# Performance work log

Hardware: AMD Instinct MI355X
Metric: run time of the kernel (lower is better)

Reference implementation:

```python
import jax, jax.numpy as jnp
import numpy as np
import math

N_ENTITIES = 200000
N_ITEMS = 100000
N_REL = 40
DIM = 64
N_HEADS = 2
DK = DIM // N_HEADS
N_EDGES = 1500000
K_EDGES = 256
K_ITEMS = 100


def setup_inputs() -> dict:
    key = jax.random.key(0)
    k1, k2, k3, k4, k5, k6 = jax.random.split(key, 6)
    entity_emb = jax.random.normal(k1, (N_ENTITIES, DIM), jnp.float32) * 0.1
    W_Q = jax.random.normal(k2, (DIM, DIM), jnp.float32) * (1.0 / math.sqrt(DIM))
    relation_emb = jax.random.normal(k3, (N_REL - 1, DIM), jnp.float32) * 0.1
    edge_index = jax.random.randint(k4, (2, N_EDGES), 0, N_ENTITIES, jnp.int32)
    # edge_type in [1, N_REL-1]: code indexes relation_emb[edge_type - 1]
    edge_type = jax.random.randint(k5, (N_EDGES,), 1, N_REL, jnp.int32)
    # uniform(0,1) driving the gumbel noise -log(-log(u)); clipped away from 0
    noise_u = jax.random.uniform(k6, (N_EDGES,), jnp.float32, 1e-9, 1.0)
    return {"entity_emb": entity_emb, "W_Q": W_Q, "relation_emb": relation_emb,
            "noise_u": noise_u, "edge_index": edge_index, "edge_type": edge_type}


def reference(entity_emb, W_Q, relation_emb, noise_u, edge_index, edge_type):
    head, tail = edge_index[0], edge_index[1]
    E = edge_index.shape[1]

    # --- norm_attn_computer (AttnHGCN): per-edge multi-head attention ---
    # project once on nodes, then gather (same math as (emb[head] @ W_Q))
    proj = entity_emb @ W_Q                               # [N, D]
    q = proj[head].reshape(E, N_HEADS, DK)                # [E, H, Dk]
    k = proj[tail].reshape(E, N_HEADS, DK)                # [E, H, Dk]
    rel = relation_emb[edge_type - 1].reshape(E, N_HEADS, DK)
    attn = jnp.sum(q * k * rel, axis=-1) / math.sqrt(DK)  # [E, H]
    edge_attn_logits = attn.mean(axis=-1)                 # [E]

    # scatter_softmax over head nodes, then multiply by head degree (norm)
    seg_max = jax.lax.stop_gradient(
        jax.ops.segment_max(edge_attn_logits, head, num_segments=N_ENTITIES))
    ex = jnp.exp(edge_attn_logits - seg_max[head])
    denom = jax.ops.segment_sum(ex, head, num_segments=N_ENTITIES)
    edge_attn_score = ex / denom[head]
    deg = jax.ops.segment_sum(jnp.ones_like(edge_attn_logits), head,
                              num_segments=N_ENTITIES)
    edge_attn_score = edge_attn_score * deg[head]         # [E]

    # --- attn logit sums per item (head + tail scatter_sum), topk 100 ---
    sum_by_node = (jax.ops.segment_sum(edge_attn_logits, head, num_segments=N_ENTITIES)
                   + jax.ops.segment_sum(edge_attn_logits, tail, num_segments=N_ENTITIES))
    top_items_v, top_attn_items = jax.lax.top_k(sum_by_node[:N_ITEMS], K_ITEMS)

    # --- gumbel-noise injection + edge topk 256 ---
    noisy_score = edge_attn_score + (-jnp.log(-jnp.log(noise_u)))
    topk_v, topk_attn_edge_id = jax.lax.top_k(noisy_score, K_EDGES)

    return (edge_attn_score, topk_v, topk_attn_edge_id, top_items_v, top_attn_items)
```

## Files before the change

### kernel.cpp

```cpp
#include <hip/hip_runtime.h>

#define N_ENTITIES 200000
#define N_ITEMS    100000
#define DIM        64
#define N_EDGES    1500000
#define K_EDGES    256
#define K_ITEMS    100
#define SCALE      0.08838834764831845f

#define CAND_CAP   8192
#define NSCANB     ((N_ENTITIES + 255) / 256)
#define NXCD       8

typedef unsigned long long u64;


__device__ __forceinline__ unsigned xcd_atomic_add(unsigned* p, unsigned v) {
    return __hip_atomic_fetch_add(p, v, __ATOMIC_RELAXED, __HIP_MEMORY_SCOPE_WORKGROUP);
}
__device__ __forceinline__ void xcd_atomic_addf(float* p, float v) {
    __hip_atomic_fetch_add(p, v, __ATOMIC_RELAXED, __HIP_MEMORY_SCOPE_WORKGROUP);
}

__device__ __forceinline__ unsigned fkey(float x) {
    unsigned u = __float_as_uint(x);
    return (u & 0x80000000u) ? ~u : (u | 0x80000000u);
}
__device__ __forceinline__ float funkey(unsigned k) {
    return (k & 0x80000000u) ? __uint_as_float(k & 0x7fffffffu)
                             : __uint_as_float(~k);
}

__device__ __forceinline__ void lds_hist_add(unsigned* h, unsigned bin, bool valid, int lane) {
    bool need = valid;
    for (;;) {
        unsigned long long mask = __ballot(need);
        if (mask == 0ull) break;
        int leader = __ffsll(mask) - 1;
        unsigned lbin = __shfl(bin, leader, 64);
        bool same = need && (bin == lbin);
        unsigned long long grp = __ballot(same);
        if (lane == leader) atomicAdd(&h[lbin], (unsigned)__popcll(grp));
        need = need && !same;
    }
}

__device__ __forceinline__ unsigned select_digit(const unsigned* __restrict__ hist,
                                                 unsigned Keff, unsigned* above) {
    unsigned cum = 0;
    int b = 255;
    for (; b > 0; --b) {
        unsigned hb = hist[b];
        if (cum + hb >= Keff) break;
        cum += hb;
    }
    *above = cum;
    return (unsigned)b;
}

__global__ __launch_bounds__(256) void proj_kernel(const float* __restrict__ emb,
                                                   const float* __restrict__ W,
                                                   float* __restrict__ proj,
                                                   const int* __restrict__ head,
                                                   unsigned* __restrict__ degiX,
                                                   unsigned* __restrict__ rank) {
    unsigned xcd;
    asm volatile("s_getreg_b32 %0, hwreg(HW_REG_XCC_ID)" : "=s"(xcd));
    xcd &= (NXCD - 1);

    int e = blockIdx.x * blockDim.x + threadIdx.x;
    unsigned rk = 0;
    bool haveEdge = (e < N_EDGES);
    if (haveEdge)
        rk = (xcd << 28) | xcd_atomic_add(&degiX[(size_t)xcd * N_ENTITIES + head[e]], 1u);

    __shared__ float part[4][16][64];
    const int t = threadIdx.x;
    const int c = t & 63;
    const int q = __builtin_amdgcn_readfirstlane(t >> 6);

    float Wreg[16];
#pragma unroll
    for (int j = 0; j < 16; ++j) Wreg[j] = W[(q * 16 + j) * 64 + c];

    const int base = blockIdx.x * 16;
    const float* erow = emb + (size_t)base * 64 + q * 16;

    float acc[16];
#pragma unroll
    for (int r = 0; r < 16; ++r) acc[r] = 0.f;
#pragma unroll
    for (int r = 0; r < 16; ++r) {
#pragma unroll
        for (int j = 0; j < 16; ++j)
            acc[r] += erow[r * 64 + j] * Wreg[j];
    }
#pragma unroll
    for (int r = 0; r < 16; ++r) part[q][r][c] = acc[r];
    __syncthreads();
#pragma unroll
    for (int it = 0; it < 4; ++it) {
        int oi = t + it * 256;
        int r = oi >> 6, cc = oi & 63;
        float s = part[0][r][cc] + part[1][r][cc] + part[2][r][cc] + part[3][r][cc];
        proj[(size_t)(base + r) * 64 + cc] = s;
    }
    if (haveEdge) rank[e] = rk;
}

__global__ void scan1_kernel(unsigned* __restrict__ degiX,
                             unsigned* __restrict__ degtot,
                             unsigned* __restrict__ start,
                             unsigned* __restrict__ bsum) {
    __shared__ unsigned s[256];
    int t = threadIdx.x, i = blockIdx.x * 256 + t;
    unsigned tot = 0;
    if (i < N_ENTITIES) {
        unsigned px[NXCD];
#pragma unroll
        for (int x = 0; x < NXCD; ++x) {
            px[x] = tot;
            tot += degiX[(size_t)x * N_ENTITIES + i];
        }
#pragma unroll
        for (int x = 0; x < NXCD; ++x)
            degiX[(size_t)x * N_ENTITIES + i] = px[x];
        degtot[i] = tot;
    }
    s[t] = tot;
    __syncthreads();
    for (int off = 1; off < 256; off <<= 1) {
        unsigned x = s[t];
        unsigned y = (t >= off) ? s[t - off] : 0u;
        __syncthreads();
        s[t] = x + y;
        __syncthreads();
    }
    if (i < N_ENTITIES) start[i] = s[t] - tot;
    if (t == 255) bsum[blockIdx.x] = s[t];
}

__global__ __launch_bounds__(256) void scan23_kernel(const unsigned* __restrict__ bsum,
                                                     unsigned* __restrict__ start,
                                                     unsigned* __restrict__ degiX) {
    __shared__ unsigned part[4];
    const int b = blockIdx.x;
    const int t = threadIdx.x;
    unsigned s = 0;
    for (int j = t; j < b; j += 256) s += bsum[j];
#pragma unroll
    for (int off = 1; off < 64; off <<= 1) s += __shfl_xor(s, off, 64);
    if ((t & 63) == 0) part[t >> 6] = s;
    __syncthreads();
    unsigned prefix = part[0] + part[1] + part[2] + part[3];
    int i = b * 256 + t;
    if (i < N_ENTITIES) {
        unsigned sg = start[i] + prefix;
        start[i] = sg;
#pragma unroll
        for (int x = 0; x < NXCD; ++x)
            degiX[(size_t)x * N_ENTITIES + i] += sg;
    }
}

__global__ void scatter_kernel(const int* __restrict__ head, const int* __restrict__ tail,
                               const int* __restrict__ etype,
                               unsigned* __restrict__ rank,
                               const unsigned* __restrict__ startX,
                               u64* __restrict__ rec, int csrMode) {
    int i = blockIdx.x * blockDim.x + threadIdx.x;
    if (i >= N_EDGES) return;
    unsigned r = rank[i];
    unsigned x = r >> 28;
    unsigned slot = startX[(size_t)x * N_ENTITIES + head[i]] + (r & 0x0FFFFFFFu);
    u64 R = ((u64)(unsigned)tail[i] << 27) | ((u64)(unsigned)(etype[i] - 1) << 21) | (u64)(unsigned)i;
    rec[slot] = R;
    if (csrMode) rank[i] = slot;
}

__global__ __launch_bounds__(256) void node_pass(const float4* __restrict__ proj4,
                                                 const float4* __restrict__ rel4,
                                                 const u64* __restrict__ rec,
                                                 const unsigned* __restrict__ start,
                                                 const unsigned* __restrict__ degtot,
                                                 float* __restrict__ logitsOut,
                                                 int csrMode,
                                                 float2* __restrict__ nd,
                                                 float* __restrict__ sumhead,
                                                 float* __restrict__ sumtailR,
                                                 int repMask) {
    unsigned xcd;
    asm volatile("s_getreg_b32 %0, hwreg(HW_REG_XCC_ID)" : "=s"(xcd));
    float* st = sumtailR + (size_t)(xcd & (unsigned)repMask) * N_ITEMS;
    const bool xcdLocal = (repMask == NXCD - 1);

    int wave = (blockIdx.x * blockDim.x + threadIdx.x) >> 6;
    int lane = threadIdx.x & 63;
    int slot = lane >> 4, sl = lane & 15;
    unsigned s = start[wave], len = degtot[wave];
    float4 ph = proj4[(size_t)wave * 16 + sl];
    float dsum = 0.f, lsum = 0.f;
    for (unsigned k0 = 0; k0 < len; k0 += 8) {
        unsigned ka = k0 + slot, kb = ka + 4;
        bool va = (ka < len), vb = (kb < len);
        u64 Ra = rec[s + (va ? ka : 0u)];
        u64 Rb = rec[s + (vb ? kb : 0u)];
        unsigned ta = (unsigned)(Ra >> 27), ria = ((unsigned)(Ra >> 21)) & 63u;
        unsigned tb = (unsigned)(Rb >> 27), rib = ((unsigned)(Rb >> 21)) & 63u;
        unsigned ea = (unsigned)Ra & 0x1FFFFFu, eb = (unsigned)Rb & 0x1FFFFFu;
        float4 pa = proj4[(size_t)ta * 16 + sl];
        float4 qa = rel4[(size_t)ria * 16 + sl];
        float4 pb = proj4[(size_t)tb * 16 + sl];
        float4 qb = rel4[(size_t)rib * 16 + sl];
        float xa = ph.x * pa.x * qa.x + ph.y * pa.y * qa.y + ph.z * pa.z * qa.z + ph.w * pa.w * qa.w;
        float xb = ph.x * pb.x * qb.x + ph.y * pb.y * qb.y + ph.z * pb.z * qb.z + ph.w * pb.w * qb.w;
        xa += __shfl_xor(xa, 1, 64);  xb += __shfl_xor(xb, 1, 64);
        xa += __shfl_xor(xa, 2, 64);  xb += __shfl_xor(xb, 2, 64);
        xa += __shfl_xor(xa, 4, 64);  xb += __shfl_xor(xb, 4, 64);
        xa += __shfl_xor(xa, 8, 64);  xb += __shfl_xor(xb, 8, 64);
        if (sl == 0) {
            if (va) {
                float lg = xa * SCALE;
                logitsOut[csrMode ? (s + ka) : ea] = lg;
                dsum += __expf(lg);
                lsum += lg;
                if (ta < N_ITEMS) {
                    if (xcdLocal) xcd_atomic_addf(&st[ta], lg);
                    else          atomicAdd(&st[ta], lg);
                }
            }
            if (vb) {
                float lg = xb * SCALE;
                logitsOut[csrMode ? (s + kb) : eb] = lg;
                dsum += __expf(lg);
                lsum += lg;
                if (tb < N_ITEMS) {
                    if (xcdLocal) xcd_atomic_addf(&st[tb], lg);
                    else          atomicAdd(&st[tb], lg);
                }
            }
        }
    }
    dsum += __shfl_xor(dsum, 16, 64);
    dsum += __shfl_xor(dsum, 32, 64);
    lsum += __shfl_xor(lsum, 16, 64);
    lsum += __shfl_xor(lsum, 32, 64);
    if (lane == 0) {
        nd[wave] = make_float2(dsum, (float)len);
        sumhead[wave] = lsum;
    }
}

__global__ void edge_pass3(const float* __restrict__ logitsEdge,
                           const float* __restrict__ logitsCsr,
                           const unsigned* __restrict__ slotmap, int csrMode,
                           const int* __restrict__ head,
                           const float2* __restrict__ nd, const float* __restrict__ noise_u,
                           const float* __restrict__ sumhead, const float* __restrict__ sumtailR,
                           int R,
                           float* __restrict__ out_scores, unsigned* __restrict__ keysE,
                           unsigned* __restrict__ keysI, unsigned* __restrict__ hists) {
    __shared__ unsigned hE[256];
    __shared__ unsigned hI[256];
    for (int j = threadIdx.x; j < 256; j += blockDim.x) { hE[j] = 0; hI[j] = 0; }
    __syncthreads();
    int i = blockIdx.x * blockDim.x + threadIdx.x;
    int lane = threadIdx.x & 63;

    unsigned bin = 0;
    bool valid = (i < N_EDGES);
    if (valid) {
        float lg = csrMode ? logitsCsr[slotmap[i]] : logitsEdge[i];
        float2 dd = nd[head[i]];
        float score = __expf(lg) / dd.x * dd.y;
        out_scores[i] = score;
        float noise = -logf(-logf(noise_u[i]));
        unsigned k = fkey(score + noise);
        keysE[i] = k;
        bin = k >> 24;
    }
    lds_hist_add(hE, bin, valid, lane);

    bin = 0;
    valid = (i < N_ITEMS);
    if (valid) {
        float s = sumhead[i];
        for (int r = 0; r < R; ++r) s += sumtailR[(size_t)r * N_ITEMS + i];
        unsigned k = fkey(s);
        keysI[i] = k;
        bin = k >> 24;
    }
    lds_hist_add(hI, bin, valid, lane);

    __syncthreads();
    for (int j = threadIdx.x; j < 256; j += blockDim.x) {
        unsigned v = hE[j];
        if (v) atomicAdd(&hists[j], v);
        v = hI[j];
        if (v) atomicAdd(&hists[3 * 256 + j], v);
    }
}

__global__ void collect_kernel(const unsigned* __restrict__ keysE,
                               const unsigned* __restrict__ keysI,
                               const unsigned* __restrict__ hists,
                               unsigned* __restrict__ counters, unsigned* __restrict__ cand) {
    const int y = blockIdx.y;
    const unsigned* keys = y ? keysI : keysE;
    const int n = y ? N_ITEMS : N_EDGES;
    const unsigned K = y ? K_ITEMS : K_EDGES;
    const unsigned* H = hists + (size_t)y * 3 * 256;
    unsigned aboveA;
    unsigned binA = select_digit(H, K, &aboveA);
    const unsigned T = binA << 24;
    unsigned* cd = cand + (size_t)y * 2 * CAND_CAP;

    int i = blockIdx.x * blockDim.x + threadIdx.x;
    int stride = gridDim.x * blockDim.x;
    for (; i < n; i += stride) {
        unsigned k = keys[i];
        if (k >= T) {
            unsigned p = atomicAdd(&counters[y], 1u);
            if (p < (unsigned)CAND_CAP) { cd[2 * p] = k; cd[2 * p + 1] = (unsigned)i; }
        }
    }
}

__global__ void final_topk_kernel(const unsigned* __restrict__ cand,
                                  const unsigned* __restrict__ counters,
                                  float* __restrict__ out_topkv, float* __restrict__ out_topki,
                                  float* __restrict__ out_itemv, float* __restrict__ out_itemi) {
    __shared__ unsigned sk[CAND_CAP];
    __shared__ unsigned si[CAND_CAP];
    const int y = blockIdx.x;
    const int K = y ? K_ITEMS : K_EDGES;
    float* outv = y ? out_itemv : out_topkv;
    float* outi = y ? out_itemi : out_topki;
    const unsigned* cd = cand + (size_t)y * 2 * CAND_CAP;
    unsigned m = counters[y];
    if (m > (unsigned)CAND_CAP) m = CAND_CAP;
    for (unsigned i = threadIdx.x; i < m; i += blockDim.x) {
        sk[i] = cd[2 * i];
        si[i] = cd[2 * i + 1];
    }
    __syncthreads();
    for (unsigned i = threadIdx.x; i < m; i += blockDim.x) {
        unsigned ki = sk[i], xi = si[i];
        int r = 0;
        for (unsigned j = 0; j < m; ++j) {
            unsigned kj = sk[j];
            if (kj > ki || (kj == ki && si[j] < xi)) r++;
        }
        if (r < K) {
            outv[r] = funkey(ki);
            outi[r] = (float)xi;
        }
    }
}

extern "C" void kernel_launch(void* const* d_in, const int* in_sizes, int n_in,
                              void* d_out, int out_size, void* d_ws, size_t ws_size,
                              hipStream_t stream) {
    (void)in_sizes; (void)n_in; (void)out_size;
    const float* emb    = (const float*)d_in[0];
    const float* W      = (const float*)d_in[1];
    const float* rel    = (const float*)d_in[2];
    const float* noise  = (const float*)d_in[3];
    const int*   eidx   = (const int*)d_in[4];
    const int*   etype  = (const int*)d_in[5];
    const int* head = eidx;
    const int* tail = eidx + N_EDGES;

    float* out        = (float*)d_out;
    float* out_scores = out;
    float* out_topkv  = out + N_EDGES;
    float* out_topki  = out + N_EDGES + K_EDGES;
    float* out_itemv  = out + N_EDGES + 2 * K_EDGES;
    float* out_itemi  = out + N_EDGES + 2 * K_EDGES + K_ITEMS;

    auto layout_floats = [](int R, int csr) -> size_t {
        return (size_t)N_ENTITIES * DIM + N_EDGES + 2 * (size_t)N_EDGES
             + N_ENTITIES + (size_t)NXCD * N_ENTITIES + N_ENTITIES
             + (size_t)R * N_ITEMS
             + 2 * 3 * 256 + 2 + 2 * (size_t)N_ENTITIES + N_ENTITIES
             + 1024 + 2 * 2 * CAND_CAP + (csr ? (size_t)N_EDGES : 0);
    };
    int R = 8, csr = 1;
    while (R > 1 && ws_size < layout_floats(R, 1) * 4) R >>= 1;
    if (ws_size < layout_floats(1, 1) * 4) {
        csr = 0;
        R = 8;
        while (R > 1 && ws_size < layout_floats(R, 0) * 4) R >>= 1;
    }

    float* ws = (float*)d_ws;
    size_t o = 0;
    float*    proj    = ws + o;               o += (size_t)N_ENTITIES * DIM;
    unsigned* rank    = (unsigned*)(ws + o);
    float*    logits  = ws + o;               o += N_EDGES;
    u64*      rec     = (u64*)(ws + o);       o += 2 * (size_t)N_EDGES;
    unsigned* keysE   = (unsigned*)rec;
    unsigned* keysI   = keysE + N_EDGES;
    unsigned* start   = (unsigned*)(ws + o);  o += N_ENTITIES;
    unsigned* degtot  = (unsigned*)(ws + o);  o += N_ENTITIES;
    unsigned* degiX   = (unsigned*)(ws + o);  o += (size_t)NXCD * N_ENTITIES;
    float*    sumtailR= ws + o;               o += (size_t)R * N_ITEMS;
    unsigned* hists   = (unsigned*)(ws + o);  o += 2 * 3 * 256;
    unsigned* counters= (unsigned*)(ws + o);  o += 2;
    float2*   nd      = (float2*)(ws + o);    o += 2 * (size_t)N_ENTITIES;
    float*    sumhead = ws + o;               o += N_ENTITIES;
    unsigned* bsum    = (unsigned*)(ws + o);  o += 1024;
    unsigned* cand    = (unsigned*)(ws + o);  o += 2 * 2 * CAND_CAP;
    float*    logitsCsr = ws + o;             if (csr) o += N_EDGES;

    float*    nodePassLogits = csr ? logitsCsr : logits;

    hipMemsetAsync(degiX, 0,
                   ((size_t)NXCD * N_ENTITIES + (size_t)R * N_ITEMS + 2 * 3 * 256 + 2) * 4,
                   stream);
    hipLaunchKernelGGL(proj_kernel, dim3(12500), dim3(256), 0, stream,
                       emb, W, proj, head, degiX, rank);
    hipLaunchKernelGGL(scan1_kernel, dim3(NSCANB), dim3(256), 0, stream,
                       degiX, degtot, start, bsum);
    hipLaunchKernelGGL(scan23_kernel, dim3(NSCANB), dim3(256), 0, stream,
                       bsum, start, degiX);
    hipLaunchKernelGGL(scatter_kernel, dim3((N_EDGES + 255) / 256), dim3(256), 0, stream,
                       head, tail, etype, rank, degiX, rec, csr);
    hipLaunchKernelGGL(node_pass, dim3(N_ENTITIES / 4), dim3(256), 0, stream,
                       (const float4*)proj, (const float4*)rel, rec, start, degtot,
                       nodePassLogits, csr, nd, sumhead, sumtailR, R - 1);
    hipLaunchKernelGGL(edge_pass3, dim3((N_EDGES + 255) / 256), dim3(256), 0, stream,
                       logits, logitsCsr, rank, csr, head, (const float2*)nd, noise,
                       sumhead, sumtailR, R,
                       out_scores, keysE, keysI, hists);
    hipLaunchKernelGGL(collect_kernel, dim3(512, 2), dim3(256), 0, stream,
                       keysE, keysI, hists, counters, cand);
    hipLaunchKernelGGL(final_topk_kernel, dim3(2), dim3(1024), 0, stream,
                       cand, counters, out_topkv, out_topki, out_itemv, out_itemi);
}
```

Measured before the change: 508.5 us.

## Use grid-stride edge pass with per-block histograms and separate reduction kernel

The edge pass now runs as a fixed grid of 1024 blocks with a grid-stride loop and plain LDS atomics in place of the ballot-based aggregation. Each block writes its 512-bin histogram to its own workspace row, and a new small kernel reduces the rows. This removes global histogram atomics and the memset of the histogram region. The XCD-local float atomic in node_pass is also replaced with an inline-asm global_atomic_add_f32, which could change atomic scope semantics. The cost is an extra kernel launch and more workspace.

```diff
diff --git a/kernel.cpp b/kernel.cpp
--- a/kernel.cpp
+++ b/kernel.cpp
@@ -11,15 +11,16 @@
 #define CAND_CAP   8192
 #define NSCANB     ((N_ENTITIES + 255) / 256)
 #define NXCD       8
+#define NBLK3      1024
 
 typedef unsigned long long u64;
 
 
+__device__ __forceinline__ void l2_atomic_add_f32(float* p, float v) {
+    asm volatile("global_atomic_add_f32 %0, %1, off" :: "v"(p), "v"(v) : "memory");
+}
 __device__ __forceinline__ unsigned xcd_atomic_add(unsigned* p, unsigned v) {
     return __hip_atomic_fetch_add(p, v, __ATOMIC_RELAXED, __HIP_MEMORY_SCOPE_WORKGROUP);
-}
-__device__ __forceinline__ void xcd_atomic_addf(float* p, float v) {
-    __hip_atomic_fetch_add(p, v, __ATOMIC_RELAXED, __HIP_MEMORY_SCOPE_WORKGROUP);
 }
 
 __device__ __forceinline__ unsigned fkey(float x) {
@@ -29,20 +30,6 @@
 __device__ __forceinline__ float funkey(unsigned k) {
     return (k & 0x80000000u) ? __uint_as_float(k & 0x7fffffffu)
                              : __uint_as_float(~k);
-}
-
-__device__ __forceinline__ void lds_hist_add(unsigned* h, unsigned bin, bool valid, int lane) {
-    bool need = valid;
-    for (;;) {
-        unsigned long long mask = __ballot(need);
-        if (mask == 0ull) break;
-        int leader = __ffsll(mask) - 1;
-        unsigned lbin = __shfl(bin, leader, 64);
-        bool same = need && (bin == lbin);
-        unsigned long long grp = __ballot(same);
-        if (lane == leader) atomicAdd(&h[lbin], (unsigned)__popcll(grp));
-        need = need && !same;
-    }
 }
 
 __device__ __forceinline__ unsigned select_digit(const unsigned* __restrict__ hist,
@@ -225,7 +212,7 @@
                 dsum += __expf(lg);
                 lsum += lg;
                 if (ta < N_ITEMS) {
-                    if (xcdLocal) xcd_atomic_addf(&st[ta], lg);
+                    if (xcdLocal) l2_atomic_add_f32(&st[ta], lg);
                     else          atomicAdd(&st[ta], lg);
                 }
             }
@@ -235,7 +222,7 @@
                 dsum += __expf(lg);
                 lsum += lg;
                 if (tb < N_ITEMS) {
-                    if (xcdLocal) xcd_atomic_addf(&st[tb], lg);
+                    if (xcdLocal) l2_atomic_add_f32(&st[tb], lg);
                     else          atomicAdd(&st[tb], lg);
                 }
             }
@@ -251,7 +238,7 @@
     }
 }
 
-__global__ void edge_pass3(const float* __restrict__ logitsEdge,
+__global__ __launch_bounds__(256) void edge_pass3(const float* __restrict__ logitsEdge,
                            const float* __restrict__ logitsCsr,
                            const unsigned* __restrict__ slotmap, int csrMode,
                            const int* __restrict__ head,
@@ -259,17 +246,13 @@
                            const float* __restrict__ sumhead, const float* __restrict__ sumtailR,
                            int R,
                            float* __restrict__ out_scores, unsigned* __restrict__ keysE,
-                           unsigned* __restrict__ keysI, unsigned* __restrict__ hists) {
-    __shared__ unsigned hE[256];
-    __shared__ unsigned hI[256];
-    for (int j = threadIdx.x; j < 256; j += blockDim.x) { hE[j] = 0; hI[j] = 0; }
-    __syncthreads();
-    int i = blockIdx.x * blockDim.x + threadIdx.x;
-    int lane = threadIdx.x & 63;
-
-    unsigned bin = 0;
-    bool valid = (i < N_EDGES);
-    if (valid) {
+                           unsigned* __restrict__ keysI, unsigned* __restrict__ histB) {
+    __shared__ unsigned hh[512];
+    for (int j = threadIdx.x; j < 512; j += blockDim.x) hh[j] = 0;
+    __syncthreads();
+
+    const int stride = NBLK3 * 256;
+    for (int i = blockIdx.x * blockDim.x + threadIdx.x; i < N_EDGES; i += stride) {
         float lg = csrMode ? logitsCsr[slotmap[i]] : logitsEdge[i];
         float2 dd = nd[head[i]];
         float score = __expf(lg) / dd.x * dd.y;
@@ -277,28 +260,29 @@
         float noise = -logf(-logf(noise_u[i]));
         unsigned k = fkey(score + noise);
         keysE[i] = k;
-        bin = k >> 24;
-    }
-    lds_hist_add(hE, bin, valid, lane);
-
-    bin = 0;
-    valid = (i < N_ITEMS);
-    if (valid) {
-        float s = sumhead[i];
-        for (int r = 0; r < R; ++r) s += sumtailR[(size_t)r * N_ITEMS + i];
-        unsigned k = fkey(s);
-        keysI[i] = k;
-        bin = k >> 24;
-    }
-    lds_hist_add(hI, bin, valid, lane);
-
-    __syncthreads();
-    for (int j = threadIdx.x; j < 256; j += blockDim.x) {
-        unsigned v = hE[j];
-        if (v) atomicAdd(&hists[j], v);
-        v = hI[j];
-        if (v) atomicAdd(&hists[3 * 256 + j], v);
-    }
+        atomicAdd(&hh[k >> 24], 1u);
+        if (i < N_ITEMS) {
+            float s = sumhead[i];
+            for (int r = 0; r < R; ++r) s += sumtailR[(size_t)r * N_ITEMS + i];
+            unsigned ki = fkey(s);
+            keysI[i] = ki;
+            atomicAdd(&hh[256 + (ki >> 24)], 1u);
+        }
+    }
+    __syncthreads();
+    unsigned* row = histB + (size_t)blockIdx.x * 512;
+    for (int j = threadIdx.x; j < 512; j += blockDim.x) row[j] = hh[j];
+}
+
+__global__ void reduce_hist_kernel(const unsigned* __restrict__ histB,
+                                   unsigned* __restrict__ hists) {
+    const int bin = blockIdx.x;
+    unsigned s = 0;
+    for (int r = threadIdx.x; r < NBLK3; r += 64)
+        s += histB[(size_t)r * 512 + bin];
+#pragma unroll
+    for (int off = 1; off < 64; off <<= 1) s += __shfl_xor(s, off, 64);
+    if (threadIdx.x == 0) hists[bin] = s;
 }
 
 __global__ void collect_kernel(const unsigned* __restrict__ keysE,
@@ -309,7 +293,7 @@
     const unsigned* keys = y ? keysI : keysE;
     const int n = y ? N_ITEMS : N_EDGES;
     const unsigned K = y ? K_ITEMS : K_EDGES;
-    const unsigned* H = hists + (size_t)y * 3 * 256;
+    const unsigned* H = hists + (size_t)y * 256;
     unsigned aboveA;
     unsigned binA = select_digit(H, K, &aboveA);
     const unsigned T = binA << 24;
@@ -380,9 +364,10 @@
 
     auto layout_floats = [](int R, int csr) -> size_t {
         return (size_t)N_ENTITIES * DIM + N_EDGES + 2 * (size_t)N_EDGES
-             + N_ENTITIES + (size_t)NXCD * N_ENTITIES + N_ENTITIES
-             + (size_t)R * N_ITEMS
-             + 2 * 3 * 256 + 2 + 2 * (size_t)N_ENTITIES + N_ENTITIES
+             + N_ENTITIES + N_ENTITIES + (size_t)NXCD * N_ENTITIES
+             + (size_t)R * N_ITEMS + 2
+             + (size_t)NBLK3 * 512 + 512
+             + 2 * (size_t)N_ENTITIES + N_ENTITIES
              + 1024 + 2 * 2 * CAND_CAP + (csr ? (size_t)N_EDGES : 0);
     };
     int R = 8, csr = 1;
@@ -405,8 +390,9 @@
     unsigned* degtot  = (unsigned*)(ws + o);  o += N_ENTITIES;
     unsigned* degiX   = (unsigned*)(ws + o);  o += (size_t)NXCD * N_ENTITIES;
     float*    sumtailR= ws + o;               o += (size_t)R * N_ITEMS;
-    unsigned* hists   = (unsigned*)(ws + o);  o += 2 * 3 * 256;
     unsigned* counters= (unsigned*)(ws + o);  o += 2;
+    unsigned* histB   = (unsigned*)(ws + o);  o += (size_t)NBLK3 * 512;
+    unsigned* hists   = (unsigned*)(ws + o);  o += 512;
     float2*   nd      = (float2*)(ws + o);    o += 2 * (size_t)N_ENTITIES;
     float*    sumhead = ws + o;               o += N_ENTITIES;
     unsigned* bsum    = (unsigned*)(ws + o);  o += 1024;
@@ -416,8 +402,7 @@
     float*    nodePassLogits = csr ? logitsCsr : logits;
 
     hipMemsetAsync(degiX, 0,
-                   ((size_t)NXCD * N_ENTITIES + (size_t)R * N_ITEMS + 2 * 3 * 256 + 2) * 4,
-                   stream);
+                   ((size_t)NXCD * N_ENTITIES + (size_t)R * N_ITEMS + 2) * 4, stream);
     hipLaunchKernelGGL(proj_kernel, dim3(12500), dim3(256), 0, stream,
                        emb, W, proj, head, degiX, rank);
     hipLaunchKernelGGL(scan1_kernel, dim3(NSCANB), dim3(256), 0, stream,
@@ -429,10 +414,11 @@
     hipLaunchKernelGGL(node_pass, dim3(N_ENTITIES / 4), dim3(256), 0, stream,
                        (const float4*)proj, (const float4*)rel, rec, start, degtot,
                        nodePassLogits, csr, nd, sumhead, sumtailR, R - 1);
-    hipLaunchKernelGGL(edge_pass3, dim3((N_EDGES + 255) / 256), dim3(256), 0, stream,
+    hipLaunchKernelGGL(edge_pass3, dim3(NBLK3), dim3(256), 0, stream,
                        logits, logitsCsr, rank, csr, head, (const float2*)nd, noise,
                        sumhead, sumtailR, R,
-                       out_scores, keysE, keysI, hists);
+                       out_scores, keysE, keysI, histB);
+    hipLaunchKernelGGL(reduce_hist_kernel, dim3(512), dim3(64), 0, stream, histB, hists);
     hipLaunchKernelGGL(collect_kernel, dim3(512, 2), dim3(256), 0, stream,
                        keysE, keysI, hists, counters, cand);
     hipLaunchKernelGGL(final_topk_kernel, dim3(2), dim3(1024), 0, stream,
```

Result: faster. 465.1 us (-8.5%).
